# Kernel tuning notes

Measured on AMD Instinct MI355X. Metric: run time of the kernel, lower is better.

Reference implementation:

```python
import jax, jax.numpy as jnp
import numpy as np

EPS = 1e-5        # BatchNorm1d default eps
SLOPE = 0.01      # torch LeakyReLU default negative slope


def setup_inputs() -> dict:
    key = jax.random.key(0)
    ks = jax.random.split(key, 10)
    N3, N2, N1, N0 = 4096, 16384, 65536, 262144  # coarse -> fine point hierarchy
    return {
        "feats": jax.random.normal(ks[0], (N3, 258), jnp.float32),
        "skip1": jax.random.normal(ks[1], (N0, 128), jnp.float32),
        "skip2": jax.random.normal(ks[2], (N1, 256), jnp.float32),
        "skip3": jax.random.normal(ks[3], (N2, 512), jnp.float32),
        "idx1": jax.random.randint(ks[4], (N2,), 0, N3, jnp.int32),
        "idx2": jax.random.randint(ks[5], (N1,), 0, N2, jnp.int32),
        "idx3": jax.random.randint(ks[6], (N0,), 0, N1, jnp.int32),
        "W1": jax.random.normal(ks[7], (770, 129), jnp.float32) * 0.05,
        "b1": jnp.zeros((129,), jnp.float32),
        "g1": jnp.ones((129,), jnp.float32),
        "be1": jnp.zeros((129,), jnp.float32),
        "W2": jax.random.normal(ks[8], (385, 64), jnp.float32) * 0.05,
        "b2": jnp.zeros((64,), jnp.float32),
        "g2": jnp.ones((64,), jnp.float32),
        "be2": jnp.zeros((64,), jnp.float32),
        "W3": jax.random.normal(ks[9], (192, 34), jnp.float32) * 0.05,
        "b3": jnp.zeros((34,), jnp.float32),
    }


def _bn(y, g, b):
    # training-mode batch norm over the points dimension (biased variance)
    m = y.mean(axis=0)
    v = y.var(axis=0)
    return (y - m) * jax.lax.rsqrt(v + EPS) * g + b


def _lrelu(x):
    return jnp.where(x >= 0, x, SLOPE * x)


def reference(feats, skip1, skip2, skip3, idx1, idx2, idx3,
              W1, b1, g1, be1, W2, b2, g2, be2, W3, b3):
    # stage 1: nearest upsample N3->N2, concat skip3, conv1x1 + BN + LeakyReLU
    x = jnp.concatenate([feats[idx1], skip3], axis=1)        # [N2, 770]
    x = _lrelu(_bn(x @ W1 + b1, g1, be1))                    # [N2, 129]
    # stage 2: upsample N2->N1
    x = jnp.concatenate([x[idx2], skip2], axis=1)            # [N1, 385]
    x = _lrelu(_bn(x @ W2 + b2, g2, be2))                    # [N1, 64]
    # stage 3: upsample N1->N0, plain conv1x1 (no BN / no activation)
    x = jnp.concatenate([x[idx3], skip1], axis=1)            # [N0, 192]
    return x @ W3 + b3                                       # [N0, 34]
```

## Files before the change

### kernel.cpp

```cpp
#include <hip/hip_runtime.h>

#define EPS 1e-5f
#define SLOPE 0.01f

typedef __attribute__((ext_vector_type(4))) float f32x4;
typedef __attribute__((ext_vector_type(8))) short bf16x8;

__device__ __forceinline__ short f2bf(float f) {
    unsigned u = __float_as_uint(f);
    unsigned r = (u + 0x7FFFu + ((u >> 16) & 1u)) >> 16;
    return (short)r;
}
__device__ __forceinline__ float bf2f(short h) {
    return __uint_as_float(((unsigned)(unsigned short)h) << 16);
}
__device__ __forceinline__ float lrelu(float v) { return v >= 0.f ? v : SLOPE * v; }

__device__ __forceinline__ void gload16(const void* g, float* l) {
    __builtin_amdgcn_global_load_lds(
        (const __attribute__((address_space(1))) unsigned*)g,
        (__attribute__((address_space(3))) unsigned*)l, 16, 0, 0);
}
__device__ __forceinline__ void gload4(const void* g, float* l) {
    __builtin_amdgcn_global_load_lds(
        (const __attribute__((address_space(1))) unsigned*)g,
        (__attribute__((address_space(3))) unsigned*)l, 4, 0, 0);
}

#define WCASE(N) case N: asm volatile("s_waitcnt vmcnt(" #N ")" ::: "memory"); break;
__device__ __forceinline__ void wait_vm(int n) {
    switch (n) {
    WCASE(0) WCASE(1) WCASE(2) WCASE(3) WCASE(4) WCASE(5) WCASE(6) WCASE(7)
    WCASE(8) WCASE(9) WCASE(10) WCASE(11) WCASE(12) WCASE(13) WCASE(14) WCASE(15)
    WCASE(16) WCASE(17) WCASE(18) WCASE(19) WCASE(20) WCASE(21) WCASE(22) WCASE(23)
    WCASE(24) WCASE(25) WCASE(26) WCASE(27) WCASE(28) WCASE(29) WCASE(30) WCASE(31)
    WCASE(32) WCASE(33) WCASE(34) WCASE(35) WCASE(36) WCASE(37) WCASE(38) WCASE(39)
    WCASE(40) WCASE(41) WCASE(42) WCASE(43) WCASE(44) WCASE(45) WCASE(46) WCASE(47)
    WCASE(48) WCASE(49) WCASE(50) WCASE(51) WCASE(52) WCASE(53) WCASE(54) WCASE(55)
    WCASE(56) WCASE(57) WCASE(58) WCASE(59) WCASE(60) WCASE(61) WCASE(62) WCASE(63)
    default: asm volatile("s_waitcnt vmcnt(0)" ::: "memory"); break;
    }
}

__device__ __forceinline__ int swz_cf(int s, int r) {
    return ((((s >> 1) ^ r) & 7) << 1) | (s & 1);
}

__global__ void prep(const float* __restrict__ W1, const float* __restrict__ W2,
                     const float* __restrict__ W3,
                     short* __restrict__ Wt1, short* __restrict__ Wt2,
                     short* __restrict__ Wt3, float* __restrict__ stats,
                     short* __restrict__ y1h)
{
    const int id0 = blockIdx.x * 256 + threadIdx.x;
    const int str = gridDim.x * 256;
    for (int id = id0; id < 4096; id += str) stats[id] = 0.f;
    for (int id = id0; id < 26 * 9 * 512; id += str) {
        int e = id & 7, ln = (id >> 3) & 63, g = id >> 9;
        int t = g / 9, nt = g - t * 9;
        int kv = t * 32 + (ln >> 4) * 8 + e;
        int n  = nt * 16 + (ln & 15);
        float v = 0.f; int ks = -1;
        if (kv < 258) ks = kv; else if (kv >= 320) ks = kv - 62;
        if (ks >= 0 && ks < 770 && n < 129) v = W1[ks * 129 + n];
        Wt1[id] = f2bf(v);
    }
    for (int id = id0; id < 14 * 4 * 512; id += str) {
        int e = id & 7, ln = (id >> 3) & 63, g = id >> 9;
        int t = g >> 2, nt = g & 3;
        int kv = t * 32 + (ln >> 4) * 8 + e;
        int n  = nt * 16 + (ln & 15);
        float v = 0.f; int ks = -1;
        if (kv < 129) ks = kv; else if (kv >= 192) ks = kv - 63;
        if (ks >= 0 && ks < 385) v = W2[ks * 64 + n];
        Wt2[id] = f2bf(v);
    }
    for (int id = id0; id < 6 * 3 * 512; id += str) {
        int e = id & 7, ln = (id >> 3) & 63, g = id >> 9;
        int t = g / 3, nt = g - t * 3;
        int kv = t * 32 + (ln >> 4) * 8 + e;
        int n  = nt * 16 + (ln & 15);
        float v = (n < 34) ? W3[kv * 34 + n] : 0.f;
        Wt3[id] = f2bf(v);
    }
    for (int id = id0; id < 16384 * 64; id += str)
        y1h[(size_t)(id >> 6) * 192 + 128 + (id & 63)] = 0;
}

template<int XD, int SD, int NCX, int NCS, int NT, int NVALID, int ODe,
         int XMODE, int XCLAMP, int BNC, int BNSTR, bool STATS, int BMODE, int MINW,
         bool OUTBF>
__global__ __launch_bounds__(256, MINW)
void mfma_stage(const void* __restrict__ xsrcv, const float* __restrict__ skip,
                const int* __restrict__ idx, const short* __restrict__ Wt,
                const float* __restrict__ bias,
                const float* __restrict__ bnsum, const float* __restrict__ bnsq,
                const float* __restrict__ bng, const float* __restrict__ bnbe,
                float invN, void* __restrict__ outv,
                float* __restrict__ ssum, float* __restrict__ ssq)
{
    constexpr int NC = NCX + NCS;
    constexpr bool BN = (BNC > 0);
    constexpr int NPAD = NT * 16;

    __shared__ __align__(16) float abuf[4][3][1024];
    __shared__ __align__(16) float bnl[BN ? 2 * NCX * 64 : 4];

    const int tid  = threadIdx.x;
    const int wave = tid >> 6, lane = tid & 63;
    const int lr = lane & 15;
    const int kg = lane >> 4;
    const int row0w = (blockIdx.x * 4 + wave) * 16;
    const short* wtf = Wt + (lane << 3);
    float* awave = &abuf[wave][0][0];

    if (BN) {
        for (int i = tid; i < NCX * 64; i += 256) {
            float sc = 0.f, sh = 0.f;
            if (i < BNC) {
                float s = 0.f, q = 0.f;
#pragma unroll
                for (int p = 0; p < 8; ++p) {
                    s += bnsum[p * BNSTR + i];
                    q += bnsq[p * BNSTR + i];
                }
                float m   = s * invN;
                float var = fmaf(-m, m, q * invN);
                float rs  = rsqrtf(var + EPS);
                sc = rs * bng[i];
                sh = fmaf(-m, sc, bnbe[i]);
            }
            bnl[i] = sc;
            bnl[NCX * 64 + i] = sh;
        }
        __syncthreads();
    }

    const float* prowf[XMODE == 0 ? 16 : 1];
    const short* prowh[XMODE == 2 ? 2 : 1];
    if constexpr (XMODE == 0) {
#pragma unroll
        for (int j = 0; j < 16; ++j)
            prowf[j] = (const float*)xsrcv + (size_t)idx[row0w + j] * XD;
    } else {
#pragma unroll
        for (int i = 0; i < 2; ++i)
            prowh[i] = (const short*)xsrcv
                       + (size_t)idx[row0w + i * 8 + (lane >> 3)] * XD;
    }

    auto sD = [](int c) -> int {
        if (c < 0 || c >= NC) return 0;
        if (c < NCX) return (XMODE == 0) ? 16 : 2;
        return 4;
    };
    auto sB = [](int c) -> int {
        if (c < 0 || c >= NC) return 0;
        return 2 * NT;
    };

    auto issue = [&](int c) {
        float* wb = awave + (c % 3) * 1024;
        if (c < NCX) {
            if constexpr (XMODE == 2) {
#pragma unroll
                for (int i = 0; i < 2; ++i) {
                    const int r  = i * 8 + (lane >> 3);
                    const int ss = (lane & 7) ^ (r & 7);
                    gload16(prowh[i] + c * 64 + ss * 8, wb + i * 256);
                }
            } else {
#pragma unroll
                for (int j = 0; j < 16; ++j) {
                    const int cf = swz_cf(lane >> 2, j);
                    int col = c * 64 + cf * 4 + (lane & 3);
                    if (XCLAMP > 0 && c == NCX - 1) col = min(col, XCLAMP - 1);
                    gload4(prowf[j] + col, wb + j * 64);
                }
            }
        } else {
            const int jc = c - NCX;
#pragma unroll
            for (int q = 0; q < 4; ++q) {
                const int rl = q * 4 + kg;
                const int cf = swz_cf(lane & 15, rl);
                gload16(skip + (size_t)(row0w + rl) * SD + jc * 64 + cf * 4,
                        wb + q * 256);
            }
        }
    };

    bf16x8 Bp[(BMODE == 2) ? 2 * NC * NT : 1];
    bf16x8 Bf[(BMODE == 1) ? 3 : 1][2][NT];
    auto loadB = [&](int cc) {
#pragma unroll
        for (int tt = 0; tt < 2; ++tt)
#pragma unroll
            for (int nt = 0; nt < NT; ++nt)
                Bf[cc % 3][tt][nt] =
                    *(const bf16x8*)(wtf + (((2 * cc + tt) * NT + nt) << 9));
    };

    f32x4 acc[NT];
#pragma unroll
    for (int nt = 0; nt < NT; ++nt) acc[nt] = (f32x4){0.f, 0.f, 0.f, 0.f};

    if constexpr (BMODE == 2) {
#pragma unroll
        for (int tv = 0; tv < 2 * NC; ++tv)
#pragma unroll
            for (int nt = 0; nt < NT; ++nt)
                Bp[tv * NT + nt] = *(const bf16x8*)(wtf + ((tv * NT + nt) << 9));
    }

    issue(0);
    if constexpr (BMODE == 1) loadB(0);
    if (NC > 1) issue(1);
    if constexpr (BMODE == 1) { if (NC > 1) loadB(1); }

#pragma unroll
    for (int c = 0; c < NC; ++c) {
        if (c + 2 < NC) issue(c + 2);
        int w;
        if constexpr (BMODE == 0)      w = sD(c+1) + sD(c+2) + sB(c-1) + sB(c-2);
        else if constexpr (BMODE == 1) w = sD(c+1) + sD(c+2) + sB(c) + sB(c+1);
        else                           w = sD(c+1) + sD(c+2);
        wait_vm(w > 63 ? 63 : w);
        if constexpr (BMODE == 1) { if (c + 2 < NC) loadB(c + 2); }

        const float* wb = awave + (c % 3) * 1024;
#pragma unroll
        for (int tt = 0; tt < 2; ++tt) {
            bf16x8 a;
            if (c < NCX && XMODE == 2) {
                const short* hp = (const short*)wb + lr * 64
                                  + (((tt * 4 + kg) ^ (lr & 7)) << 3);
                bf16x8 ar = *(const bf16x8*)hp;
                if (BN) {
                    const int kb = c * 64 + tt * 32 + kg * 8;
                    f32x4 c0 = *(const f32x4*)&bnl[kb];
                    f32x4 c1 = *(const f32x4*)&bnl[kb + 4];
                    f32x4 h0 = *(const f32x4*)&bnl[NCX * 64 + kb];
                    f32x4 h1 = *(const f32x4*)&bnl[NCX * 64 + kb + 4];
#pragma unroll
                    for (int e = 0; e < 4; ++e) {
                        a[e]     = f2bf(lrelu(fmaf(bf2f(ar[e]),     c0[e], h0[e])));
                        a[e + 4] = f2bf(lrelu(fmaf(bf2f(ar[e + 4]), c1[e], h1[e])));
                    }
                } else {
                    a = ar;
                }
            } else {
                const int p0 = tt * 4 + kg;
                const float* fp = wb + lr * 64 + ((p0 ^ (lr & 7)) << 3);
                f32x4 lo = *(const f32x4*)fp;
                f32x4 hi = *(const f32x4*)(fp + 4);
                float v[8];
#pragma unroll
                for (int e = 0; e < 4; ++e) { v[e] = lo[e]; v[e + 4] = hi[e]; }
#pragma unroll
                for (int e = 0; e < 8; ++e) a[e] = f2bf(v[e]);
            }
#pragma unroll
            for (int nt = 0; nt < NT; ++nt) {
                bf16x8 b;
                if constexpr (BMODE == 2)      b = Bp[(2 * c + tt) * NT + nt];
                else if constexpr (BMODE == 1) b = Bf[c % 3][tt][nt];
                else b = *(const bf16x8*)(wtf + (((2 * c + tt) * NT + nt) << 9));
                acc[nt] = __builtin_amdgcn_mfma_f32_16x16x32_bf16(a, b, acc[nt], 0, 0, 0);
            }
        }
    }

#pragma unroll
    for (int nt = 0; nt < NT; ++nt) {
        const int n = nt * 16 + lr;
        const float bv = (n < NVALID) ? bias[n] : 0.f;
#pragma unroll
        for (int r = 0; r < 4; ++r) acc[nt][r] += bv;
        if (n < NVALID) {
#pragma unroll
            for (int r = 0; r < 4; ++r) {
                const size_t o = (size_t)(row0w + kg * 4 + r) * ODe + n;
                if constexpr (OUTBF) ((short*)outv)[o] = f2bf(acc[nt][r]);
                else                 ((float*)outv)[o] = acc[nt][r];
            }
        }
    }

    if constexpr (STATS) {
        float* ls = &abuf[0][0][0];
        __syncthreads();
        for (int i = tid; i < 2 * NPAD; i += 256) ls[i] = 0.f;
        __syncthreads();
#pragma unroll
        for (int nt = 0; nt < NT; ++nt) {
            float s = acc[nt][0] + acc[nt][1] + acc[nt][2] + acc[nt][3];
            float q = acc[nt][0]*acc[nt][0] + acc[nt][1]*acc[nt][1]
                    + acc[nt][2]*acc[nt][2] + acc[nt][3]*acc[nt][3];
            s += __shfl_xor(s, 16, 64);
            s += __shfl_xor(s, 32, 64);
            q += __shfl_xor(q, 16, 64);
            q += __shfl_xor(q, 32, 64);
            if (lane < 16) {
                atomicAdd(&ls[nt * 16 + lr], s);
                atomicAdd(&ls[NPAD + nt * 16 + lr], q);
            }
        }
        __syncthreads();
        const int part = blockIdx.x & 7;
        for (int i = tid; i < NPAD; i += 256) {
            atomicAdd(&ssum[part * NPAD + i], ls[i]);
            atomicAdd(&ssq[part * NPAD + i], ls[NPAD + i]);
        }
    }
}

extern "C" void kernel_launch(void* const* d_in, const int* in_sizes, int n_in,
                              void* d_out, int out_size, void* d_ws, size_t ws_size,
                              hipStream_t stream) {
    const float* feats = (const float*)d_in[0];
    const float* skip1 = (const float*)d_in[1];
    const float* skip2 = (const float*)d_in[2];
    const float* skip3 = (const float*)d_in[3];
    const int*   idx1  = (const int*)d_in[4];
    const int*   idx2  = (const int*)d_in[5];
    const int*   idx3  = (const int*)d_in[6];
    const float* W1    = (const float*)d_in[7];
    const float* b1    = (const float*)d_in[8];
    const float* g1    = (const float*)d_in[9];
    const float* be1   = (const float*)d_in[10];
    const float* W2    = (const float*)d_in[11];
    const float* b2    = (const float*)d_in[12];
    const float* g2    = (const float*)d_in[13];
    const float* be2   = (const float*)d_in[14];
    const float* W3    = (const float*)d_in[15];
    const float* b3    = (const float*)d_in[16];

    float* ws   = (float*)d_ws;
    float* sum1 = ws;
    float* sq1  = ws + 1152;
    float* sum2 = ws + 2304;
    float* sq2  = ws + 2816;
    short* Wt1  = (short*)(ws + 4096);
    short* Wt2  = Wt1 + 119808;
    short* Wt3  = Wt2 + 28672;
    short* y1h  = Wt3 + 9216;
    short* y2h  = y1h + (size_t)16384 * 192;
    float* outp = (float*)d_out;

    prep<<<512, 256, 0, stream>>>(W1, W2, W3, Wt1, Wt2, Wt3, ws, y1h);

    mfma_stage<258, 512, 5, 8, 9, 129, 192, 0, 258, 0, 1, true, 0, 2, true>
        <<<256, 256, 0, stream>>>(feats, skip3, idx1, Wt1, b1,
                                  nullptr, nullptr, nullptr, nullptr, 0.f,
                                  y1h, sum1, sq1);

    mfma_stage<192, 256, 3, 4, 4, 64, 64, 2, 0, 129, 144, true, 1, 3, true>
        <<<1024, 256, 0, stream>>>(y1h, skip2, idx2, Wt2, b2,
                                   sum1, sq1, g1, be1, 1.f / 16384.f,
                                   y2h, sum2, sq2);

    mfma_stage<64, 128, 1, 2, 3, 34, 34, 2, 0, 64, 64, false, 2, 3, false>
        <<<4096, 256, 0, stream>>>(y2h, skip1, idx3, Wt3, b3,
                                   sum2, sq2, g2, be2, 1.f / 65536.f,
                                   outp, nullptr, nullptr);
}
```

Baseline: 104.3 us.

## Pre-convert feats to padded bf16 and tile multiple row blocks per wave in stage 3

The prep kernel now converts feats to a bf16 table padded to 320 columns, so stage 1 gathers them with 16-byte loads instead of 16 per-row 4-byte fp32 loads. The gather path becomes uniform bf16 for every stage. A new NTILE parameter lets each wave process several 16-row tiles in one continuous load/MFMA pipeline. Stage 3 uses two tiles per wave with half the grid, which spreads the prologue and B-fragment preload over more rows. Zero-filling the y1h pad columns is dropped, and the output is now written after each tile.

```diff
diff --git a/kernel.cpp b/kernel.cpp
--- a/kernel.cpp
+++ b/kernel.cpp
@@ -20,11 +20,6 @@
     __builtin_amdgcn_global_load_lds(
         (const __attribute__((address_space(1))) unsigned*)g,
         (__attribute__((address_space(3))) unsigned*)l, 16, 0, 0);
-}
-__device__ __forceinline__ void gload4(const void* g, float* l) {
-    __builtin_amdgcn_global_load_lds(
-        (const __attribute__((address_space(1))) unsigned*)g,
-        (__attribute__((address_space(3))) unsigned*)l, 4, 0, 0);
 }
 
 #define WCASE(N) case N: asm volatile("s_waitcnt vmcnt(" #N ")" ::: "memory"); break;
@@ -47,10 +42,10 @@
 }
 
 __global__ void prep(const float* __restrict__ W1, const float* __restrict__ W2,
-                     const float* __restrict__ W3,
+                     const float* __restrict__ W3, const float* __restrict__ feats,
                      short* __restrict__ Wt1, short* __restrict__ Wt2,
-                     short* __restrict__ Wt3, float* __restrict__ stats,
-                     short* __restrict__ y1h)
+                     short* __restrict__ Wt3, short* __restrict__ featsh,
+                     float* __restrict__ stats)
 {
     const int id0 = blockIdx.x * 256 + threadIdx.x;
     const int str = gridDim.x * 256;
@@ -83,15 +78,17 @@
         float v = (n < 34) ? W3[kv * 34 + n] : 0.f;
         Wt3[id] = f2bf(v);
     }
-    for (int id = id0; id < 16384 * 64; id += str)
-        y1h[(size_t)(id >> 6) * 192 + 128 + (id & 63)] = 0;
+    for (int id = id0; id < 4096 * 320; id += str) {
+        int r = id / 320, c = id - r * 320;
+        featsh[id] = f2bf(c < 258 ? feats[r * 258 + c] : 0.f);
+    }
 }
 
 template<int XD, int SD, int NCX, int NCS, int NT, int NVALID, int ODe,
-         int XMODE, int XCLAMP, int BNC, int BNSTR, bool STATS, int BMODE, int MINW,
-         bool OUTBF>
+         int BNC, int BNSTR, bool STATS, int BMODE, int MINW, bool OUTBF,
+         int NTILE>
 __global__ __launch_bounds__(256, MINW)
-void mfma_stage(const void* __restrict__ xsrcv, const float* __restrict__ skip,
+void mfma_stage(const short* __restrict__ xsrc, const float* __restrict__ skip,
                 const int* __restrict__ idx, const short* __restrict__ Wt,
                 const float* __restrict__ bias,
                 const float* __restrict__ bnsum, const float* __restrict__ bnsq,
@@ -100,6 +97,7 @@
                 float* __restrict__ ssum, float* __restrict__ ssq)
 {
     constexpr int NC = NCX + NCS;
+    constexpr int TCC = NTILE * NC;
     constexpr bool BN = (BNC > 0);
     constexpr int NPAD = NT * 16;
 
@@ -110,7 +108,7 @@
     const int wave = tid >> 6, lane = tid & 63;
     const int lr = lane & 15;
     const int kg = lane >> 4;
-    const int row0w = (blockIdx.x * 4 + wave) * 16;
+    const int row0w = (blockIdx.x * 4 + wave) * (16 * NTILE);
     const short* wtf = Wt + (lane << 3);
     float* awave = &abuf[wave][0][0];
 
@@ -136,47 +134,32 @@
         __syncthreads();
     }
 
-    const float* prowf[XMODE == 0 ? 16 : 1];
-    const short* prowh[XMODE == 2 ? 2 : 1];
-    if constexpr (XMODE == 0) {
-#pragma unroll
-        for (int j = 0; j < 16; ++j)
-            prowf[j] = (const float*)xsrcv + (size_t)idx[row0w + j] * XD;
-    } else {
+    const short* prowh[NTILE][2];
+#pragma unroll
+    for (int t = 0; t < NTILE; ++t)
 #pragma unroll
         for (int i = 0; i < 2; ++i)
-            prowh[i] = (const short*)xsrcv
-                       + (size_t)idx[row0w + i * 8 + (lane >> 3)] * XD;
-    }
-
-    auto sD = [](int c) -> int {
-        if (c < 0 || c >= NC) return 0;
-        if (c < NCX) return (XMODE == 0) ? 16 : 2;
-        return 4;
+            prowh[t][i] = xsrc
+                + (size_t)idx[row0w + t * 16 + i * 8 + (lane >> 3)] * XD;
+
+    auto sDg = [](int cc) -> int {
+        if (cc < 0 || cc >= TCC) return 0;
+        return ((cc % NC) < NCX) ? 2 : 4;
     };
-    auto sB = [](int c) -> int {
-        if (c < 0 || c >= NC) return 0;
+    auto sBg = [](int cc) -> int {
+        if (cc < 0 || cc >= TCC) return 0;
         return 2 * NT;
     };
 
-    auto issue = [&](int c) {
-        float* wb = awave + (c % 3) * 1024;
+    auto issue = [&](int cc) {
+        float* wb = awave + (cc % 3) * 1024;
+        const int t = cc / NC, c = cc % NC;
         if (c < NCX) {
-            if constexpr (XMODE == 2) {
-#pragma unroll
-                for (int i = 0; i < 2; ++i) {
-                    const int r  = i * 8 + (lane >> 3);
-                    const int ss = (lane & 7) ^ (r & 7);
-                    gload16(prowh[i] + c * 64 + ss * 8, wb + i * 256);
-                }
-            } else {
-#pragma unroll
-                for (int j = 0; j < 16; ++j) {
-                    const int cf = swz_cf(lane >> 2, j);
-                    int col = c * 64 + cf * 4 + (lane & 3);
-                    if (XCLAMP > 0 && c == NCX - 1) col = min(col, XCLAMP - 1);
-                    gload4(prowf[j] + col, wb + j * 64);
-                }
+#pragma unroll
+            for (int i = 0; i < 2; ++i) {
+                const int r  = i * 8 + (lane >> 3);
+                const int ss = (lane & 7) ^ (r & 7);
+                gload16(prowh[t][i] + c * 64 + ss * 8, wb + i * 256);
             }
         } else {
             const int jc = c - NCX;
@@ -184,7 +167,7 @@
             for (int q = 0; q < 4; ++q) {
                 const int rl = q * 4 + kg;
                 const int cf = swz_cf(lane & 15, rl);
-                gload16(skip + (size_t)(row0w + rl) * SD + jc * 64 + cf * 4,
+                gload16(skip + (size_t)(row0w + t * 16 + rl) * SD + jc * 64 + cf * 4,
                         wb + q * 256);
             }
         }
@@ -201,10 +184,6 @@
                     *(const bf16x8*)(wtf + (((2 * cc + tt) * NT + nt) << 9));
     };
 
-    f32x4 acc[NT];
-#pragma unroll
-    for (int nt = 0; nt < NT; ++nt) acc[nt] = (f32x4){0.f, 0.f, 0.f, 0.f};
-
     if constexpr (BMODE == 2) {
 #pragma unroll
         for (int tv = 0; tv < 2 * NC; ++tv)
@@ -215,24 +194,33 @@
 
     issue(0);
     if constexpr (BMODE == 1) loadB(0);
-    if (NC > 1) issue(1);
+    if (TCC > 1) issue(1);
     if constexpr (BMODE == 1) { if (NC > 1) loadB(1); }
 
-#pragma unroll
-    for (int c = 0; c < NC; ++c) {
-        if (c + 2 < NC) issue(c + 2);
-        int w;
-        if constexpr (BMODE == 0)      w = sD(c+1) + sD(c+2) + sB(c-1) + sB(c-2);
-        else if constexpr (BMODE == 1) w = sD(c+1) + sD(c+2) + sB(c) + sB(c+1);
-        else                           w = sD(c+1) + sD(c+2);
+    f32x4 acc[NT];
+
+#pragma unroll
+    for (int cc = 0; cc < TCC; ++cc) {
+        const int t = cc / NC, c = cc % NC;
+        if (c == 0) {
+#pragma unroll
+            for (int nt = 0; nt < NT; ++nt) acc[nt] = (f32x4){0.f, 0.f, 0.f, 0.f};
+        }
+        if (cc + 2 < TCC) issue(cc + 2);
+        int w = sDg(cc + 1) + sDg(cc + 2);
+        if constexpr (BMODE == 0) w += sBg(cc - 1) + sBg(cc - 2);
+        if constexpr (BMODE == 1) w += sBg(cc) + sBg(cc + 1);
+        if constexpr (NTILE > 1) {
+            if ((c == 0 && cc >= NC) || (c == 1 && cc >= NC + 1)) w += 4 * NT;
+        }
         wait_vm(w > 63 ? 63 : w);
-        if constexpr (BMODE == 1) { if (c + 2 < NC) loadB(c + 2); }
-
-        const float* wb = awave + (c % 3) * 1024;
+        if constexpr (BMODE == 1) { if (cc + 2 < TCC) loadB(cc + 2); }
+
+        const float* wb = awave + (cc % 3) * 1024;
 #pragma unroll
         for (int tt = 0; tt < 2; ++tt) {
             bf16x8 a;
-            if (c < NCX && XMODE == 2) {
+            if (c < NCX) {
                 const short* hp = (const short*)wb + lr * 64
                                   + (((tt * 4 + kg) ^ (lr & 7)) << 3);
                 bf16x8 ar = *(const bf16x8*)hp;
@@ -255,35 +243,37 @@
                 const float* fp = wb + lr * 64 + ((p0 ^ (lr & 7)) << 3);
                 f32x4 lo = *(const f32x4*)fp;
                 f32x4 hi = *(const f32x4*)(fp + 4);
-                float v[8];
-#pragma unroll
-                for (int e = 0; e < 4; ++e) { v[e] = lo[e]; v[e + 4] = hi[e]; }
-#pragma unroll
-                for (int e = 0; e < 8; ++e) a[e] = f2bf(v[e]);
+#pragma unroll
+                for (int e = 0; e < 4; ++e) {
+                    a[e]     = f2bf(lo[e]);
+                    a[e + 4] = f2bf(hi[e]);
+                }
             }
 #pragma unroll
             for (int nt = 0; nt < NT; ++nt) {
                 bf16x8 b;
                 if constexpr (BMODE == 2)      b = Bp[(2 * c + tt) * NT + nt];
-                else if constexpr (BMODE == 1) b = Bf[c % 3][tt][nt];
+                else if constexpr (BMODE == 1) b = Bf[cc % 3][tt][nt];
                 else b = *(const bf16x8*)(wtf + (((2 * c + tt) * NT + nt) << 9));
                 acc[nt] = __builtin_amdgcn_mfma_f32_16x16x32_bf16(a, b, acc[nt], 0, 0, 0);
             }
         }
-    }
-
-#pragma unroll
-    for (int nt = 0; nt < NT; ++nt) {
-        const int n = nt * 16 + lr;
-        const float bv = (n < NVALID) ? bias[n] : 0.f;
-#pragma unroll
-        for (int r = 0; r < 4; ++r) acc[nt][r] += bv;
-        if (n < NVALID) {
-#pragma unroll
-            for (int r = 0; r < 4; ++r) {
-                const size_t o = (size_t)(row0w + kg * 4 + r) * ODe + n;
-                if constexpr (OUTBF) ((short*)outv)[o] = f2bf(acc[nt][r]);
-                else                 ((float*)outv)[o] = acc[nt][r];
+
+        if (c == NC - 1) {
+#pragma unroll
+            for (int nt = 0; nt < NT; ++nt) {
+                const int n = nt * 16 + lr;
+                const float bv = (n < NVALID) ? bias[n] : 0.f;
+#pragma unroll
+                for (int r = 0; r < 4; ++r) acc[nt][r] += bv;
+                if (n < NVALID) {
+#pragma unroll
+                    for (int r = 0; r < 4; ++r) {
+                        const size_t o = (size_t)(row0w + t * 16 + kg * 4 + r) * ODe + n;
+                        if constexpr (OUTBF) ((short*)outv)[o] = f2bf(acc[nt][r]);
+                        else                 ((float*)outv)[o] = acc[nt][r];
+                    }
+                }
             }
         }
     }
@@ -337,32 +327,33 @@
     const float* W3    = (const float*)d_in[15];
     const float* b3    = (const float*)d_in[16];
 
-    float* ws   = (float*)d_ws;
-    float* sum1 = ws;
-    float* sq1  = ws + 1152;
-    float* sum2 = ws + 2304;
-    float* sq2  = ws + 2816;
-    short* Wt1  = (short*)(ws + 4096);
-    short* Wt2  = Wt1 + 119808;
-    short* Wt3  = Wt2 + 28672;
-    short* y1h  = Wt3 + 9216;
-    short* y2h  = y1h + (size_t)16384 * 192;
-    float* outp = (float*)d_out;
-
-    prep<<<512, 256, 0, stream>>>(W1, W2, W3, Wt1, Wt2, Wt3, ws, y1h);
-
-    mfma_stage<258, 512, 5, 8, 9, 129, 192, 0, 258, 0, 1, true, 0, 2, true>
-        <<<256, 256, 0, stream>>>(feats, skip3, idx1, Wt1, b1,
+    float* ws     = (float*)d_ws;
+    float* sum1   = ws;
+    float* sq1    = ws + 1152;
+    float* sum2   = ws + 2304;
+    float* sq2    = ws + 2816;
+    short* Wt1    = (short*)(ws + 4096);
+    short* Wt2    = Wt1 + 119808;
+    short* Wt3    = Wt2 + 28672;
+    short* featsh = Wt3 + 9216;
+    short* y1h    = featsh + 4096 * 320;
+    short* y2h    = y1h + (size_t)16384 * 192;
+    float* outp   = (float*)d_out;
+
+    prep<<<512, 256, 0, stream>>>(W1, W2, W3, feats, Wt1, Wt2, Wt3, featsh, ws);
+
+    mfma_stage<320, 512, 5, 8, 9, 129, 192, 0, 0, true, 0, 2, true, 1>
+        <<<256, 256, 0, stream>>>(featsh, skip3, idx1, Wt1, b1,
                                   nullptr, nullptr, nullptr, nullptr, 0.f,
                                   y1h, sum1, sq1);
 
-    mfma_stage<192, 256, 3, 4, 4, 64, 64, 2, 0, 129, 144, true, 1, 3, true>
+    mfma_stage<192, 256, 3, 4, 4, 64, 64, 129, 144, true, 1, 3, true, 1>
         <<<1024, 256, 0, stream>>>(y1h, skip2, idx2, Wt2, b2,
                                    sum1, sq1, g1, be1, 1.f / 16384.f,
                                    y2h, sum2, sq2);
 
-    mfma_stage<64, 128, 1, 2, 3, 34, 34, 2, 0, 64, 64, false, 2, 3, false>
-        <<<4096, 256, 0, stream>>>(y2h, skip1, idx3, Wt3, b3,
+    mfma_stage<64, 128, 1, 2, 3, 34, 34, 64, 64, false, 2, 3, false, 2>
+        <<<2048, 256, 0, stream>>>(y2h, skip1, idx3, Wt3, b3,
                                    sum2, sq2, g2, be2, 1.f / 65536.f,
                                    outp, nullptr, nullptr);
 }
```

Result: no change. 106.2 us (+1.8%).
